# Kernel optimization log

Measured on AMD Instinct MI355X. Metric: run time of the kernel, lower is better.

Reference implementation:

```python
import jax, jax.numpy as jnp
import numpy as np

DX = float(np.sqrt(512.0))  # fixed scale from the module (self.dx = sqrt(512))


def setup_inputs() -> dict:
    key = jax.random.key(0)
    ks = jax.random.split(key, 6)
    B, C, H, W = 4, 512, 64, 64
    Cq = C // 32  # reduce=32 -> 16 q/k channels
    q = jax.random.normal(ks[0], (B, C, H, W), dtype=jnp.float32)
    k = jax.random.normal(ks[1], (B, C, H, W), dtype=jnp.float32)
    v = jax.random.normal(ks[2], (B, C, H, W), dtype=jnp.float32)
    # 1x1 conv weights, kaiming-ish scale
    wq = jax.random.normal(ks[3], (Cq, C), dtype=jnp.float32) / np.sqrt(C)
    wk = jax.random.normal(ks[4], (Cq, C), dtype=jnp.float32) / np.sqrt(C)
    wv = jax.random.normal(ks[5], (C, C), dtype=jnp.float32) / np.sqrt(C)
    bq = jnp.zeros((Cq,), dtype=jnp.float32)
    bk = jnp.zeros((Cq,), dtype=jnp.float32)
    bv = jnp.zeros((C,), dtype=jnp.float32)
    return {"q": q, "k": k, "v": v, "wq": wq, "bq": bq, "wk": wk, "bk": bk, "wv": wv, "bv": bv}


def reference(q, k, v, wq, bq, wk, bk, wv, bv):
    B, C, H, W = q.shape
    N = H * W
    # 1x1 convs == per-pixel channel matmuls; flatten spatial to N tokens
    qf = q.reshape(B, C, N)
    kf = k.reshape(B, C, N)
    vf = v.reshape(B, C, N)
    proj_q = jnp.einsum('oc,bcn->bno', wq, qf) + bq  # [B, N, Cq]
    proj_k = jnp.einsum('oc,bcn->bon', wk, kf) + bk[:, None]  # [B, Cq, N]
    proj_v = jnp.einsum('oc,bcn->bon', wv, vf) + bv[:, None]  # [B, C, N]
    # energy[b,i,j] = <proj_q[b,i], proj_k[b,:,j]>
    energy = jnp.einsum('bid,bdj->bij', proj_q, proj_k)  # [B, N, N]
    attention = jax.nn.softmax(energy / DX, axis=-1)
    # out[b,c,i] = sum_j proj_v[b,c,j] * attention[b,i,j]
    out = jnp.einsum('bcj,bij->bci', proj_v, attention)
    return out.reshape(B, C, H, W) + v
```

## Files before the change

### kernel.cpp

```cpp
#include <hip/hip_runtime.h>
#include <hip/hip_bf16.h>

typedef __bf16 bf16;
typedef __bf16 bf16x8 __attribute__((ext_vector_type(8)));
typedef float f32x16 __attribute__((ext_vector_type(16)));
typedef float f32x4 __attribute__((ext_vector_type(4)));
typedef unsigned int u32x4 __attribute__((ext_vector_type(4)));

#define NB 4
#define NC 512
#define NN 4096

static constexpr float EXP2_SCALE = 0.063763926f;

static __device__ __forceinline__ unsigned pack_bf2(float a, float b){
  unsigned short ux = __builtin_bit_cast(unsigned short, (bf16)a);
  unsigned short uy = __builtin_bit_cast(unsigned short, (bf16)b);
  return (unsigned)ux | ((unsigned)uy << 16);
}

union FragU { unsigned u[4]; bf16x8 v; };

static __device__ __forceinline__ f32x16 zero16(){
  f32x16 z;
#pragma unroll
  for(int i=0;i<16;i++) z[i] = 0.0f;
  return z;
}

__global__ __launch_bounds__(256) void k_wv_cvt(const float* __restrict__ wv,
                                                bf16* __restrict__ wvL){
  int t  = blockIdx.x * 256 + threadIdx.x;
  int cg = t & 31;
  int co = t >> 5;
  const float* s = wv + (size_t)co * NC + cg * 16;
  unsigned w[8];
#pragma unroll
  for(int j=0;j<8;j++) w[j] = pack_bf2(s[2*j], s[2*j+1]);
  u32x4* d = (u32x4*)((char*)wvL + (size_t)(cg * NC + co) * 32);
  d[0] = (u32x4){w[0],w[1],w[2],w[3]};
  d[1] = (u32x4){w[4],w[5],w[6],w[7]};
}

__global__ __launch_bounds__(256) void k_v_cvt(const float* __restrict__ v,
                                               bf16* __restrict__ vL){
  int bid = blockIdx.x;
  int n  = (bid & 15) * 256 + threadIdx.x;
  int cg = (bid >> 4) & 31;
  int b  = bid >> 9;
  const float* s = v + ((size_t)(b * NC + cg * 16)) * NN + n;
  unsigned w[8];
#pragma unroll
  for(int j=0;j<8;j++) w[j] = pack_bf2(s[(size_t)(2*j)*NN], s[(size_t)(2*j+1)*NN]);
  u32x4* d = (u32x4*)((char*)vL + ((size_t)(b*32 + cg) * NN + n) * 32);
  d[0] = (u32x4){w[0],w[1],w[2],w[3]};
  d[1] = (u32x4){w[4],w[5],w[6],w[7]};
}

__global__ __launch_bounds__(256) void k_proj_qk(
    const float* __restrict__ q, const float* __restrict__ kin,
    const float* __restrict__ wq, const float* __restrict__ bq,
    const float* __restrict__ wk, const float* __restrict__ bk,
    bf16* __restrict__ Pq, bf16* __restrict__ Pk){
  __shared__ float red[4][64][20];
  int b  = blockIdx.x >> 6;
  int n0 = (blockIdx.x & 63) * 64;
  int w  = threadIdx.x >> 6;
  int lane = threadIdx.x & 63;
  const float* src = (w < 2) ? q  : kin;
  const float* wt  = (w < 2) ? wq : wk;
  int c0 = (w & 1) * 256;
  float acc[16];
#pragma unroll
  for(int o=0;o<16;o++) acc[o] = 0.0f;
  const float* sp = src + ((size_t)(b * NC + c0)) * NN + n0 + lane;
  for(int c=0;c<256;c++){
    float x = sp[(size_t)c * NN];
#pragma unroll
    for(int o=0;o<16;o++) acc[o] += wt[o * NC + c0 + c] * x;
  }
#pragma unroll
  for(int o4=0;o4<4;o4++)
    *(f32x4*)&red[w][lane][o4*4] = (f32x4){acc[o4*4],acc[o4*4+1],acc[o4*4+2],acc[o4*4+3]};
  __syncthreads();
  if(threadIdx.x < 128){
    int isk = threadIdx.x >> 6;
    int tok = threadIdx.x & 63;
    const float* bias = isk ? bk : bq;
    bf16* dst = isk ? Pk : Pq;
    int wb = isk * 2;
    unsigned wd[8];
#pragma unroll
    for(int t=0;t<8;t++){
      float a0 = red[wb][tok][2*t]   + red[wb+1][tok][2*t]   + bias[2*t];
      float a1 = red[wb][tok][2*t+1] + red[wb+1][tok][2*t+1] + bias[2*t+1];
      wd[t] = pack_bf2(a0, a1);
    }
    u32x4* d = (u32x4*)((char*)dst + ((size_t)(b * NN + n0 + tok)) * 32);
    d[0] = (u32x4){wd[0],wd[1],wd[2],wd[3]};
    d[1] = (u32x4){wd[4],wd[5],wd[6],wd[7]};
  }
}

__global__ __launch_bounds__(256) void k_proj_v(
    const bf16* __restrict__ wvL, const bf16* __restrict__ vL,
    const float* __restrict__ bv, bf16* __restrict__ PvL){
  int bid = blockIdx.x;
  int nt  = bid & 63;
  int cot = (bid >> 6) & 7;
  int b   = bid >> 9;
  int w    = threadIdx.x >> 6;
  int lane = threadIdx.x & 63;
  int l31 = lane & 31, h = lane >> 5;
  int co0 = cot * 64 + (w >> 1) * 32;
  int n0  = nt * 64 + (w & 1) * 32;
  const char* ap = (const char*)wvL + (size_t)(co0 + l31) * 32 + h * 16;
  const char* bp = (const char*)vL + ((size_t)(b * 32) * NN + n0 + l31) * 32 + h * 16;
  f32x16 acc = zero16();
  for(int kc=0;kc<32;kc++){
    bf16x8 af  = *(const bf16x8*)(ap + (size_t)kc * NC * 32);
    bf16x8 bfr = *(const bf16x8*)(bp + (size_t)kc * NN * 32);
    acc = __builtin_amdgcn_mfma_f32_32x32x16_bf16(af, bfr, acc, 0, 0, 0);
  }
  int j = n0 + l31;
  char* dbase = (char*)PvL + ((size_t)(b*256 + (j >> 4)) * NC) * 32 + (j & 15) * 2;
#pragma unroll
  for(int r=0;r<16;r++){
    int row = (r & 3) + 8 * (r >> 2) + 4 * h;
    int co = co0 + row;
    float val = acc[r] + bv[co];
    *(bf16*)(dbase + (size_t)co * 32) = (bf16)val;
  }
}

__global__ __launch_bounds__(512, 4) void k_attn(
    const bf16* __restrict__ Pq, const bf16* __restrict__ Pk,
    const bf16* __restrict__ PvL, const float* __restrict__ vin,
    float* __restrict__ out){
  __shared__ __attribute__((aligned(16))) unsigned P_lds[2][8][64][8];
  __shared__ float lsum_lds[8][64];
  int b  = blockIdx.x >> 7;
  int i0 = (blockIdx.x & 127) * 32;
  int w    = threadIdx.x >> 6;
  int lane = threadIdx.x & 63;
  int l31 = lane & 31, h = lane >> 5;
  int c0 = w * 64;

  bf16x8 qf = *(const bf16x8*)((const char*)Pq + ((size_t)(b * NN + i0 + l31)) * 32 + h * 16);

  f32x16 acc0 = zero16(), acc1 = zero16();
  float lsum = 0.0f;

  const char* pkbase = (const char*)Pk  + ((size_t)b * NN) * 32 + h * 16;
  const char* pvbase = (const char*)PvL + ((size_t)(b * 256) * NC) * 32 + h * 16;

  for(int J=0;J<16;J++){
    int buf = J & 1;
    {
      bf16x8 kf = *(const bf16x8*)(pkbase + (size_t)((J*8 + w)*32 + l31) * 32);
      f32x16 s = __builtin_amdgcn_mfma_f32_32x32x16_bf16(kf, qf, zero16(), 0, 0, 0);
      float p[16];
#pragma unroll
      for(int r=0;r<16;r++){ p[r] = exp2f(s[r] * EXP2_SCALE); lsum += p[r]; }
      unsigned qw[8], ew[8];
#pragma unroll
      for(int t=0;t<8;t++) qw[t] = pack_bf2(p[2*t], p[2*t+1]);
#pragma unroll
      for(int t=0;t<8;t++) ew[t] = (unsigned)__shfl_xor((int)qw[t], 32);
      u32x4 pa0 = h ? (u32x4){ew[2],ew[3],qw[2],qw[3]} : (u32x4){qw[0],qw[1],ew[0],ew[1]};
      u32x4 pa1 = h ? (u32x4){ew[6],ew[7],qw[6],qw[7]} : (u32x4){qw[4],qw[5],ew[4],ew[5]};
      u32x4* dst = (u32x4*)&P_lds[buf][w][lane][0];
      dst[0] = pa0;
      dst[1] = pa1;
    }
    __syncthreads();
#pragma unroll
    for(int t=0;t<8;t++){
      FragU pa0, pa1;
      const u32x4* src = (const u32x4*)&P_lds[buf][t][lane][0];
      *(u32x4*)pa0.u = src[0];
      *(u32x4*)pa1.u = src[1];
      const char* pvp = pvbase + (((size_t)(J*8 + t) * 2) * NC + c0 + l31) * 32;
      bf16x8 v00 = *(const bf16x8*)(pvp);
      bf16x8 v10 = *(const bf16x8*)(pvp + (size_t)NC * 32);
      bf16x8 v01 = *(const bf16x8*)(pvp + 1024);
      bf16x8 v11 = *(const bf16x8*)(pvp + (size_t)NC * 32 + 1024);
      acc0 = __builtin_amdgcn_mfma_f32_32x32x16_bf16(pa0.v, v00, acc0, 0, 0, 0);
      acc0 = __builtin_amdgcn_mfma_f32_32x32x16_bf16(pa1.v, v10, acc0, 0, 0, 0);
      acc1 = __builtin_amdgcn_mfma_f32_32x32x16_bf16(pa0.v, v01, acc1, 0, 0, 0);
      acc1 = __builtin_amdgcn_mfma_f32_32x32x16_bf16(pa1.v, v11, acc1, 0, 0, 0);
    }
  }
  lsum_lds[w][lane] = lsum;
  __syncthreads();
  float rowsum = 0.0f;
#pragma unroll
  for(int ww=0;ww<8;ww++) rowsum += lsum_lds[ww][l31] + lsum_lds[ww][l31 + 32];
  float rl = 1.0f / rowsum;
  float rlr[16];
#pragma unroll
  for(int r=0;r<16;r++) rlr[r] = __shfl(rl, (r & 3) + 8 * (r >> 2) + 4 * h);
#pragma unroll
  for(int cs=0;cs<2;cs++){
    f32x16 a = cs ? acc1 : acc0;
    int c = c0 + cs * 32 + l31;
    const float* vp = vin + ((size_t)(b * NC + c)) * NN + i0;
    float* op = out + ((size_t)(b * NC + c)) * NN + i0;
#pragma unroll
    for(int g=0;g<4;g++){
      int ib = 8 * g + 4 * h;
      f32x4 vv = *(const f32x4*)(vp + ib);
      f32x4 ov;
#pragma unroll
      for(int e=0;e<4;e++) ov[e] = a[4*g+e] * rlr[4*g+e] + vv[e];
      *(f32x4*)(op + ib) = ov;
    }
  }
}

extern "C" void kernel_launch(void* const* d_in, const int* in_sizes, int n_in,
                              void* d_out, int out_size, void* d_ws, size_t ws_size,
                              hipStream_t stream) {
  const float* q  = (const float*)d_in[0];
  const float* k  = (const float*)d_in[1];
  const float* v  = (const float*)d_in[2];
  const float* wq = (const float*)d_in[3];
  const float* bq = (const float*)d_in[4];
  const float* wk = (const float*)d_in[5];
  const float* bk = (const float*)d_in[6];
  const float* wv = (const float*)d_in[7];
  const float* bv = (const float*)d_in[8];
  float* out = (float*)d_out;
  char* ws = (char*)d_ws;

  bf16* Pq  = (bf16*)(ws);
  bf16* Pk  = (bf16*)(ws + (1u<<19));
  bf16* wvL = (bf16*)(ws + (2u<<19));
  bf16* vL  = (bf16*)(ws + (3u<<19));
  bf16* PvL = (bf16*)(ws + (3u<<19) + (16u<<20));

  k_wv_cvt <<<64,   256, 0, stream>>>(wv, wvL);
  k_v_cvt  <<<2048, 256, 0, stream>>>(v, vL);
  k_proj_qk<<<256,  256, 0, stream>>>(q, k, wq, bq, wk, bk, Pq, Pk);
  k_proj_v <<<2048, 256, 0, stream>>>(wvL, vL, bv, PvL);
  k_attn   <<<512,  512, 0, stream>>>(Pq, Pk, PvL, v, out);
}
```

Baseline: 341.5 us.

## Split QK projection across 8 waves, remap attention blocks per XCD, swizzle P LDS, prefetch K

The Q/K projection kernel now runs with 512 threads, so each of 8 waves reduces over 128 channels instead of 256 and the partial sums are combined through LDS. The attention kernel remaps block indices so blocks sharing a batch land on the same XCD for better L2 reuse of K/V. It also XOR-swizzles the two 16-byte halves of each P row in LDS to reduce bank conflicts, and software-prefetches the next K fragment before the softmax math. These are several unrelated tweaks that trade slightly more registers and index arithmetic for more parallelism and locality.

```diff
diff --git a/kernel.cpp b/kernel.cpp
--- a/kernel.cpp
+++ b/kernel.cpp
@@ -57,24 +57,26 @@
   d[1] = (u32x4){w[4],w[5],w[6],w[7]};
 }
 
-__global__ __launch_bounds__(256) void k_proj_qk(
+__global__ __launch_bounds__(512) void k_proj_qk(
     const float* __restrict__ q, const float* __restrict__ kin,
     const float* __restrict__ wq, const float* __restrict__ bq,
     const float* __restrict__ wk, const float* __restrict__ bk,
     bf16* __restrict__ Pq, bf16* __restrict__ Pk){
-  __shared__ float red[4][64][20];
+  __shared__ float red[8][64][20];
   int b  = blockIdx.x >> 6;
   int n0 = (blockIdx.x & 63) * 64;
   int w  = threadIdx.x >> 6;
   int lane = threadIdx.x & 63;
-  const float* src = (w < 2) ? q  : kin;
-  const float* wt  = (w < 2) ? wq : wk;
-  int c0 = (w & 1) * 256;
+  int isk = w >> 2;
+  const float* src = isk ? kin : q;
+  const float* wt  = isk ? wk : wq;
+  int c0 = (w & 3) * 128;
   float acc[16];
 #pragma unroll
   for(int o=0;o<16;o++) acc[o] = 0.0f;
   const float* sp = src + ((size_t)(b * NC + c0)) * NN + n0 + lane;
-  for(int c=0;c<256;c++){
+#pragma unroll 4
+  for(int c=0;c<128;c++){
     float x = sp[(size_t)c * NN];
 #pragma unroll
     for(int o=0;o<16;o++) acc[o] += wt[o * NC + c0 + c] * x;
@@ -84,16 +86,20 @@
     *(f32x4*)&red[w][lane][o4*4] = (f32x4){acc[o4*4],acc[o4*4+1],acc[o4*4+2],acc[o4*4+3]};
   __syncthreads();
   if(threadIdx.x < 128){
-    int isk = threadIdx.x >> 6;
+    int wk2 = threadIdx.x >> 6;
     int tok = threadIdx.x & 63;
-    const float* bias = isk ? bk : bq;
-    bf16* dst = isk ? Pk : Pq;
-    int wb = isk * 2;
+    const float* bias = wk2 ? bk : bq;
+    bf16* dst = wk2 ? Pk : Pq;
+    int wb = wk2 * 4;
     unsigned wd[8];
 #pragma unroll
     for(int t=0;t<8;t++){
-      float a0 = red[wb][tok][2*t]   + red[wb+1][tok][2*t]   + bias[2*t];
-      float a1 = red[wb][tok][2*t+1] + red[wb+1][tok][2*t+1] + bias[2*t+1];
+      float a0 = bias[2*t],  a1 = bias[2*t+1];
+#pragma unroll
+      for(int ww=0;ww<4;ww++){
+        a0 += red[wb+ww][tok][2*t];
+        a1 += red[wb+ww][tok][2*t+1];
+      }
       wd[t] = pack_bf2(a0, a1);
     }
     u32x4* d = (u32x4*)((char*)dst + ((size_t)(b * NN + n0 + tok)) * 32);
@@ -139,12 +145,16 @@
     float* __restrict__ out){
   __shared__ __attribute__((aligned(16))) unsigned P_lds[2][8][64][8];
   __shared__ float lsum_lds[8][64];
-  int b  = blockIdx.x >> 7;
-  int i0 = (blockIdx.x & 127) * 32;
+  int blk  = blockIdx.x;
+  int xcd  = blk & 7;
+  int b    = xcd >> 1;
+  int itile= ((blk >> 3) << 1) | (xcd & 1);
+  int i0 = itile * 32;
   int w    = threadIdx.x >> 6;
   int lane = threadIdx.x & 63;
   int l31 = lane & 31, h = lane >> 5;
   int c0 = w * 64;
+  int sw4 = ((lane >> 2) & 1) * 4;
 
   bf16x8 qf = *(const bf16x8*)((const char*)Pq + ((size_t)(b * NN + i0 + l31)) * 32 + h * 16);
 
@@ -153,12 +163,15 @@
 
   const char* pkbase = (const char*)Pk  + ((size_t)b * NN) * 32 + h * 16;
   const char* pvbase = (const char*)PvL + ((size_t)(b * 256) * NC) * 32 + h * 16;
+
+  bf16x8 kf = *(const bf16x8*)(pkbase + (size_t)(w * 32 + l31) * 32);
 
   for(int J=0;J<16;J++){
     int buf = J & 1;
     {
-      bf16x8 kf = *(const bf16x8*)(pkbase + (size_t)((J*8 + w)*32 + l31) * 32);
       f32x16 s = __builtin_amdgcn_mfma_f32_32x32x16_bf16(kf, qf, zero16(), 0, 0, 0);
+      if(J < 15)
+        kf = *(const bf16x8*)(pkbase + (size_t)((J+1)*8*32 + w*32 + l31) * 32);
       float p[16];
 #pragma unroll
       for(int r=0;r<16;r++){ p[r] = exp2f(s[r] * EXP2_SCALE); lsum += p[r]; }
@@ -169,17 +182,17 @@
       for(int t=0;t<8;t++) ew[t] = (unsigned)__shfl_xor((int)qw[t], 32);
       u32x4 pa0 = h ? (u32x4){ew[2],ew[3],qw[2],qw[3]} : (u32x4){qw[0],qw[1],ew[0],ew[1]};
       u32x4 pa1 = h ? (u32x4){ew[6],ew[7],qw[6],qw[7]} : (u32x4){qw[4],qw[5],ew[4],ew[5]};
-      u32x4* dst = (u32x4*)&P_lds[buf][w][lane][0];
-      dst[0] = pa0;
-      dst[1] = pa1;
+      unsigned* row = &P_lds[buf][w][lane][0];
+      *(u32x4*)(row + sw4)       = pa0;
+      *(u32x4*)(row + (4 - sw4)) = pa1;
     }
     __syncthreads();
 #pragma unroll
     for(int t=0;t<8;t++){
       FragU pa0, pa1;
-      const u32x4* src = (const u32x4*)&P_lds[buf][t][lane][0];
-      *(u32x4*)pa0.u = src[0];
-      *(u32x4*)pa1.u = src[1];
+      const unsigned* row = &P_lds[buf][t][lane][0];
+      *(u32x4*)pa0.u = *(const u32x4*)(row + sw4);
+      *(u32x4*)pa1.u = *(const u32x4*)(row + (4 - sw4));
       const char* pvp = pvbase + (((size_t)(J*8 + t) * 2) * NC + c0 + l31) * 32;
       bf16x8 v00 = *(const bf16x8*)(pvp);
       bf16x8 v10 = *(const bf16x8*)(pvp + (size_t)NC * 32);
@@ -241,7 +254,7 @@
 
   k_wv_cvt <<<64,   256, 0, stream>>>(wv, wvL);
   k_v_cvt  <<<2048, 256, 0, stream>>>(v, vL);
-  k_proj_qk<<<256,  256, 0, stream>>>(q, k, wq, bq, wk, bk, Pq, Pk);
+  k_proj_qk<<<256,  512, 0, stream>>>(q, k, wq, bq, wk, bk, Pq, Pk);
   k_proj_v <<<2048, 256, 0, stream>>>(wvL, vL, bv, PvL);
   k_attn   <<<512,  512, 0, stream>>>(Pq, Pk, PvL, v, out);
 }
```

Result: faster. 315.7 us (-7.6%).
